# Optimization experiments

Hardware: AMD Instinct MI355X
Metric: run time of the kernel (lower is better)

## Reference

```python
import jax, jax.numpy as jnp
import numpy as np

B, S, VOCAB, E, H, T = 256, 512, 50000, 256, 256, 32
PAD = VOCAB - 1  # mask = sentences != vocab_size - 1 in the original


def setup_inputs() -> dict:
    key = jax.random.key(0)
    ks = jax.random.split(key, 16)
    lengths = jnp.sort(jax.random.randint(ks[0], (B,), S // 2, S + 1))[::-1]
    lengths = lengths.at[0].set(S)  # sorted descending, max length present
    sentences = jax.random.randint(ks[1], (B, S), 0, VOCAB - 1)
    pos = jnp.arange(S)
    sentences = jnp.where(pos[None, :] < lengths[:, None], sentences, PAD)
    tags = jax.random.randint(ks[2], (B, S), 0, T)
    sc = jnp.float32(0.1)
    p = lambda k, shp: jax.random.normal(k, shp, jnp.float32) * sc
    return {
        'embed_table': p(ks[3], (VOCAB + 1, E)),
        'W_ih_f': p(ks[4], (4 * H, E)), 'W_hh_f': p(ks[5], (4 * H, H)),
        'b_ih_f': p(ks[6], (4 * H,)), 'b_hh_f': p(ks[7], (4 * H,)),
        'W_ih_b': p(ks[8], (4 * H, E)), 'W_hh_b': p(ks[9], (4 * H, H)),
        'b_ih_b': p(ks[10], (4 * H,)), 'b_hh_b': p(ks[11], (4 * H,)),
        'W_out': p(ks[12], (T, 2 * H)), 'b_out': p(ks[13], (T,)),
        'transition': jax.random.normal(ks[14], (T, T), jnp.float32),
        'sentences': sentences, 'tags': tags, 'sen_lengths': lengths,
    }


def _run_lstm(x_sbe, W_ih, W_hh, b_ih, b_hh):
    # x_sbe: [S, B, E]; torch gate order i, f, g, o
    Bsz, Hd = x_sbe.shape[1], W_hh.shape[1]
    gx = jnp.einsum('sbe,ge->sbg', x_sbe, W_ih) + b_ih + b_hh  # precompute input gates
    def step(carry, g):
        h, c = carry
        g = g + h @ W_hh.T
        i, f, gg, o = jnp.split(g, 4, axis=-1)
        c = jax.nn.sigmoid(f) * c + jax.nn.sigmoid(i) * jnp.tanh(gg)
        h = jax.nn.sigmoid(o) * jnp.tanh(c)
        return (h, c), h
    h0 = jnp.zeros((Bsz, Hd), x_sbe.dtype)
    _, hs = jax.lax.scan(step, (h0, h0), gx)
    return hs  # [S, B, H]


def _forward(embed_table, W_ih_f, W_hh_f, b_ih_f, b_hh_f,
             W_ih_b, W_hh_b, b_ih_b, b_hh_b, W_out, b_out, transition,
             sentences, tags, sen_lengths):
    mask = sentences != PAD                      # [B, S]
    x = embed_table[sentences]                   # [B, S, E]
    pos = jnp.arange(S)
    valid = pos[None, :] < sen_lengths[:, None]  # [B, S]
    # per-sequence reversal index (packed-sequence-faithful backward direction)
    idx = jnp.where(valid, sen_lengths[:, None] - 1 - pos[None, :], pos[None, :])
    h_f = _run_lstm(x.transpose(1, 0, 2), W_ih_f, W_hh_f, b_ih_f, b_hh_f).transpose(1, 0, 2)
    x_rev = jnp.take_along_axis(x, idx[:, :, None], axis=1)
    h_b = _run_lstm(x_rev.transpose(1, 0, 2), W_ih_b, W_hh_b, b_ih_b, b_hh_b).transpose(1, 0, 2)
    h_b = jnp.take_along_axis(h_b, idx[:, :, None], axis=1)
    h = jnp.concatenate([h_f, h_b], -1) * valid[:, :, None]  # pad_packed pads with zeros
    emit = h @ W_out.T + b_out                   # [B, S, T]; dropout is identity (eval)
    # ---- CRF negative log-likelihood ----
    fmask = mask.astype(emit.dtype)
    real = jnp.take_along_axis(emit, tags[:, :, None], axis=2)[..., 0]  # [B, S]
    real = real.at[:, 1:].add(transition[tags[:, :-1], tags[:, 1:]])
    real_score = (real * fmask).sum(axis=1)      # [B]
    def crf_step(alpha, inp):
        e_i, m_i = inp                           # [B, T], [B]
        scores = alpha[:, :, None] + transition[None, :, :] + e_i[:, None, :]
        new = jax.nn.logsumexp(scores, axis=1)
        return jnp.where(m_i[:, None], new, alpha), None
    alpha0 = emit[:, 0]                          # [B, T]
    xs = (emit[:, 1:].transpose(1, 0, 2), mask[:, 1:].T)
    alpha, _ = jax.lax.scan(crf_step, alpha0, xs)
    log_z = jax.nn.logsumexp(alpha, axis=1)      # [B]
    return -(real_score - log_z)                 # per-example loss [B]


def reference(embed_table, W_ih_f, W_hh_f, b_ih_f, b_hh_f,
              W_ih_b, W_hh_b, b_ih_b, b_hh_b, W_out, b_out, transition,
              sentences, tags, sen_lengths):
    return _forward(embed_table, W_ih_f, W_hh_f, b_ih_f, b_hh_f,
                    W_ih_b, W_hh_b, b_ih_b, b_hh_b, W_out, b_out, transition,
                    sentences, tags, sen_lengths)
```

## Files before the change

### kernel.cpp

```cpp
#include <hip/hip_runtime.h>
#include <hip/hip_bf16.h>


typedef __bf16 bf16x8 __attribute__((ext_vector_type(8)));
typedef float f32x4 __attribute__((ext_vector_type(4)));
typedef unsigned int uint4v __attribute__((ext_vector_type(4)));

__device__ __forceinline__ unsigned short f2bf(float f) {
  union { float f; unsigned int u; } v; v.f = f;
  unsigned int r = v.u + 0x7fffu + ((v.u >> 16) & 1u);
  return (unsigned short)(r >> 16);
}
__device__ __forceinline__ float bf2f(unsigned int lo16) {
  union { unsigned int u; float f; } v; v.u = lo16 << 16;
  return v.f;
}
__device__ __forceinline__ float fsig(float x) {
  float e = __builtin_amdgcn_exp2f(-1.4426950408889634f * x);
  return __builtin_amdgcn_rcpf(1.0f + e);
}
__device__ __forceinline__ float ftanh(float x) {
  float e = __builtin_amdgcn_exp2f(2.8853900817779268f * x);
  return 1.0f - 2.0f * __builtin_amdgcn_rcpf(e + 1.0f);
}

__device__ __forceinline__ void wait_ge(int* p, int target) {
  if (threadIdx.x == 0) {
    while (__hip_atomic_load(p, __ATOMIC_RELAXED, __HIP_MEMORY_SCOPE_AGENT) < target)
      __builtin_amdgcn_s_sleep(2);
    (void)__hip_atomic_load(p, __ATOMIC_ACQUIRE, __HIP_MEMORY_SCOPE_AGENT);
  }
  __syncthreads();
}

__device__ __forceinline__ void lds_barrier() {
  asm volatile("s_waitcnt lgkmcnt(0)\n\ts_barrier" ::: "memory");
}

__global__ void cvt_weights(const float* __restrict__ wih_f, const float* __restrict__ wih_b,
                            const float* __restrict__ whh_f, const float* __restrict__ whh_b,
                            const float* __restrict__ wo,
                            unsigned short* __restrict__ wih,
                            unsigned char* __restrict__ whh8,
                            unsigned char* __restrict__ wout8,
                            int* __restrict__ flags) {
  if (blockIdx.x == 0) {
    for (int f = threadIdx.x; f < 544; f += 256) flags[f] = 0;
  }
  int t = blockIdx.x * 256 + threadIdx.x;
  int i = t * 4;
  if (i < 524288) {
    const float* src = (i < 262144) ? wih_f : wih_b;
    f32x4 v = *(const f32x4*)(src + (i & 262143));
    uint2 p;
    p.x = f2bf(v[0]) | ((unsigned int)f2bf(v[1]) << 16);
    p.y = f2bf(v[2]) | ((unsigned int)f2bf(v[3]) << 16);
    *(uint2*)(wih + i) = p;
  } else if (i < 1048576) {
    int k = i - 524288;
    const float* src = (k < 262144) ? whh_f : whh_b;
    f32x4 v = *(const f32x4*)(src + (k & 262143));
    int r = 0;
    r = __builtin_amdgcn_cvt_pk_fp8_f32(v[0], v[1], r, false);
    r = __builtin_amdgcn_cvt_pk_fp8_f32(v[2], v[3], r, true);
    *(unsigned int*)(whh8 + k) = (unsigned int)r;
  } else if (i < 1064960) {
    int k = i - 1048576;
    f32x4 v = *(const f32x4*)(wo + k);
    int r = 0;
    r = __builtin_amdgcn_cvt_pk_fp8_f32(v[0], v[1], r, false);
    r = __builtin_amdgcn_cvt_pk_fp8_f32(v[2], v[3], r, true);
    *(unsigned int*)(wout8 + k) = (unsigned int)r;
  }
}


__device__ void gemm_role(
    const float* __restrict__ emb, const int* __restrict__ sent, const int* __restrict__ lens,
    const unsigned short* __restrict__ wih,
    const float* __restrict__ bih_f, const float* __restrict__ bhh_f,
    const float* __restrict__ bih_b, const float* __restrict__ bhh_b,
    unsigned short* __restrict__ gx, int* flags,
    unsigned short* wtile, float* btile)
{
  int gb = blockIdx.x - 32;
  int tid = threadIdx.x, w = tid >> 6, lane = tid & 63, col = lane & 15, q = lane >> 4;
  int ns = w >> 2, cg = w & 3;
  int prev_chunk = -1;

  for (int idx = gb; idx < 4096; idx += 224) {
    int k = idx >> 8, t = idx & 255;
    int ss = t >> 6, rest = t & 63;
    int dir = (rest >> 5) & 1, nc = (rest >> 2) & 7, bt = rest & 3;
    if (k != prev_chunk) {
      prev_chunk = k;
      if (k >= 2) wait_ge(&flags[512 + k - 2], 32);
    }
    int n0 = nc * 128, bbase = bt * 64;
    int sbase = k * 32 + ss * 8;

    if (sbase < lens[bbase]) {
      const unsigned short* wsrc = wih + (size_t)dir * 262144;
#pragma unroll
      for (int it = 0; it < 8; it++) {
        int seg = it * 512 + tid;
        int row = seg >> 5, kc = (seg & 31) * 8;
        *(uint4v*)(wtile + row * 264 + kc) = *(const uint4v*)(wsrc + (size_t)(n0 + row) * 256 + kc);
      }
      const float* bi = dir ? bih_b : bih_f;
      const float* bh = dir ? bhh_b : bhh_f;
      if (tid < 128) btile[tid] = bi[n0 + tid] + bh[n0 + tid];
      __syncthreads();

      bf16x8 wf[8][4];
#pragma unroll
      for (int kt = 0; kt < 8; kt++)
#pragma unroll
        for (int nt = 0; nt < 4; nt++)
          wf[kt][nt] = *(const bf16x8*)(wtile + (ns * 64 + nt * 16 + col) * 264 + kt * 32 + q * 8);
      f32x4 bias[4];
#pragma unroll
      for (int nt = 0; nt < 4; nt++)
#pragma unroll
        for (int rr = 0; rr < 4; rr++)
          bias[nt][rr] = btile[ns * 64 + nt * 16 + q * 4 + rr];

      int bidx = bbase + cg * 16 + col;
      int len = lens[bidx];
      const int* srow = sent + bidx * 512;

      for (int i = 0; i < 8; i++) {
        int s = sbase + i;
        int s_eff = dir ? ((s < len) ? (len - 1 - s) : s) : s;
        int token = srow[s_eff];
        const float* ep = emb + (size_t)token * 256;
        bf16x8 xf[8];
#pragma unroll
        for (int kt = 0; kt < 8; kt++) {
          f32x4 a0 = *(const f32x4*)(ep + kt * 32 + q * 8);
          f32x4 a1 = *(const f32x4*)(ep + kt * 32 + q * 8 + 4);
          uint4v pk;
          pk[0] = f2bf(a0[0]) | ((unsigned int)f2bf(a0[1]) << 16);
          pk[1] = f2bf(a0[2]) | ((unsigned int)f2bf(a0[3]) << 16);
          pk[2] = f2bf(a1[0]) | ((unsigned int)f2bf(a1[1]) << 16);
          pk[3] = f2bf(a1[2]) | ((unsigned int)f2bf(a1[3]) << 16);
          xf[kt] = __builtin_bit_cast(bf16x8, pk);
        }
        f32x4 acc[4];
#pragma unroll
        for (int nt = 0; nt < 4; nt++) acc[nt] = bias[nt];
#pragma unroll
        for (int kt = 0; kt < 8; kt++)
#pragma unroll
          for (int nt = 0; nt < 4; nt++)
            acc[nt] = __builtin_amdgcn_mfma_f32_16x16x32_bf16(wf[kt][nt], xf[kt], acc[nt], 0, 0, 0);
        size_t off = (size_t)(k & 1) * 16777216 + (size_t)dir * 8388608
                   + (size_t)(s - k * 32) * 262144 + (size_t)bidx * 1024 + n0 + ns * 64;
#pragma unroll
        for (int nt = 0; nt < 4; nt++) {
          uint2 pk;
          pk.x = f2bf(acc[nt][0]) | ((unsigned int)f2bf(acc[nt][1]) << 16);
          pk.y = f2bf(acc[nt][2]) | ((unsigned int)f2bf(acc[nt][3]) << 16);
          *(uint2*)(gx + off + nt * 16 + q * 4) = pk;
        }
      }
    }
    __syncthreads();
    if (tid == 0)
      __hip_atomic_fetch_add(&flags[k * 32 + ss * 8 + dir * 4 + bt], 1,
                             __ATOMIC_RELEASE, __HIP_MEMORY_SCOPE_AGENT);
  }
}

__device__ void lstm_role(
    const unsigned short* __restrict__ gx,
    const unsigned char* __restrict__ whh8,
    const unsigned char* __restrict__ wout8,
    const float* __restrict__ bout,
    const int* __restrict__ lens,
    unsigned short* __restrict__ emit_f, unsigned short* __restrict__ emit_b,
    int* flags, unsigned char (*hb4)[16 * 264])
{
  int bx = blockIdx.x;
  int dir = bx & 1, grp = bx >> 1, b0 = grp * 16;
  int bt = grp >> 2;
  int tid = threadIdx.x, w = tid >> 6, lane = tid & 63, col = lane & 15, q = lane >> 4;
  int maxlen = lens[b0];
  int bcl = b0 + col;
  int mylen = lens[bcl];

  const unsigned char* whb = whh8 + (size_t)dir * 262144;
  long wh[8][8];
#pragma unroll
  for (int kt = 0; kt < 8; kt++)
#pragma unroll
    for (int t = 0; t < 8; t++) {
      int row0 = (t & 3) * 256 + w * 32 + (t >> 2) * 16;
      wh[kt][t] = *(const long*)(whb + (size_t)(row0 + col) * 256 + kt * 32 + q * 8);
    }

  long wo8[8];
  f32x4 bo4 = (f32x4){0.f, 0.f, 0.f, 0.f};
#pragma unroll
  for (int kt = 0; kt < 8; kt++)
    wo8[kt] = *(const long*)(wout8 + (size_t)((w & 1) * 16 + col) * 512 + dir * 256 + kt * 32 + q * 8);
  if (dir == 0) {
#pragma unroll
    for (int r = 0; r < 4; r++) bo4[r] = bout[(w & 1) * 16 + q * 4 + r];
  }
  unsigned short* ebase = dir ? emit_b : emit_f;

  float c8[8];
  long hf8[8];
#pragma unroll
  for (int i = 0; i < 8; i++) { c8[i] = 0.f; hf8[i] = 0; }

  for (int c = 0; c < 16; c++) {
    int s0 = c * 32;
    if (s0 < maxlen) {
      int cend = s0 + 32; if (cend > maxlen) cend = maxlen;
      const unsigned short* gbase = gx + (size_t)(c & 1) * 16777216 + (size_t)dir * 8388608
                                       + (size_t)bcl * 1024 + q * 4;
      for (int ss = 0; ss < 4; ss++) {
        int sp0 = s0 + ss * 8;
        if (sp0 >= maxlen) break;
        int spe = sp0 + 8; if (spe > cend) spe = cend;
        wait_ge(&flags[c * 32 + ss * 8 + dir * 4 + bt], 8);

        uint2 gxr[8];
        {
          const unsigned short* gf = gbase + (size_t)(sp0 - s0) * 262144;
#pragma unroll
          for (int t = 0; t < 8; t++) {
            int row0 = (t & 3) * 256 + w * 32 + (t >> 2) * 16;
            gxr[t] = *(const uint2*)(gf + row0);
          }
        }

        for (int s = sp0; s < spe; s++) {
          f32x4 acc[8];
#pragma unroll
          for (int t = 0; t < 8; t++) {
            f32x4 a;
            a[0] = bf2f(gxr[t].x & 0xffffu); a[1] = bf2f(gxr[t].x >> 16);
            a[2] = bf2f(gxr[t].y & 0xffffu); a[3] = bf2f(gxr[t].y >> 16);
            acc[t] = a;
          }
          if (s + 1 < spe) {
            const unsigned short* gn = gbase + (size_t)(s + 1 - s0) * 262144;
#pragma unroll
            for (int t = 0; t < 8; t++) {
              int row0 = (t & 3) * 256 + w * 32 + (t >> 2) * 16;
              gxr[t] = *(const uint2*)(gn + row0);
            }
          }
#pragma unroll
          for (int kt = 0; kt < 8; kt++) {
            long hv8 = hf8[kt];
#pragma unroll
            for (int t = 0; t < 8; t++)
              acc[t] = __builtin_amdgcn_mfma_f32_16x16x32_fp8_fp8(wh[kt][t], hv8, acc[t], 0, 0, 0);
          }
          float hv[8];
#pragma unroll
          for (int a = 0; a < 2; a++)
#pragma unroll
            for (int r = 0; r < 4; r++) {
              float ig = acc[a * 4 + 0][r], fg = acc[a * 4 + 1][r];
              float gg = acc[a * 4 + 2][r], og = acc[a * 4 + 3][r];
              float cn = fsig(fg) * c8[a * 4 + r] + fsig(ig) * ftanh(gg);
              c8[a * 4 + r] = cn;
              hv[a * 4 + r] = fsig(og) * ftanh(cn);
            }
          int par = s & 7;
#pragma unroll
          for (int a = 0; a < 2; a++) {
            int r8 = 0;
            r8 = __builtin_amdgcn_cvt_pk_fp8_f32(hv[a * 4 + 0], hv[a * 4 + 1], r8, false);
            r8 = __builtin_amdgcn_cvt_pk_fp8_f32(hv[a * 4 + 2], hv[a * 4 + 3], r8, true);
            *(unsigned int*)(&hb4[par][col * 264 + w * 32 + a * 16 + q * 4]) = (unsigned int)r8;
          }
          lds_barrier();
#pragma unroll
          for (int kt = 0; kt < 8; kt++)
            hf8[kt] = *(const long*)(&hb4[par][col * 264 + kt * 32 + q * 8]);

          if ((s & 3) == 3 || s == spe - 1) {
            int ebeg = s & ~3;
            int e = ebeg + (w >> 1);
            if (e <= s) {
              f32x4 ea = bo4;
#pragma unroll
              for (int kt = 0; kt < 8; kt++) {
                long hbv = *(const long*)(&hb4[e & 7][col * 264 + kt * 32 + q * 8]);
                ea = __builtin_amdgcn_mfma_f32_16x16x32_fp8_fp8(wo8[kt], hbv, ea, 0, 0, 0);
              }
              if (e < mylen) {
                int pos = dir ? (mylen - 1 - e) : e;
                uint2 pk;
                pk.x = f2bf(ea[0]) | ((unsigned int)f2bf(ea[1]) << 16);
                pk.y = f2bf(ea[2]) | ((unsigned int)f2bf(ea[3]) << 16);
                *(uint2*)(ebase + (((size_t)bcl * 512 + pos) * 32 + (w & 1) * 16 + q * 4)) = pk;
              }
            }
          }
        }
      }
    }
    __syncthreads();
    if (tid == 0)
      __hip_atomic_fetch_add(&flags[512 + c], 1, __ATOMIC_RELEASE, __HIP_MEMORY_SCOPE_AGENT);
  }
}

__global__ __launch_bounds__(512, 2) void fused_persist(
    const float* __restrict__ emb, const int* __restrict__ sent, const int* __restrict__ lens,
    const unsigned short* __restrict__ wih,
    const float* __restrict__ bih_f, const float* __restrict__ bhh_f,
    const float* __restrict__ bih_b, const float* __restrict__ bhh_b,
    unsigned short* __restrict__ gx,
    const unsigned char* __restrict__ whh8, const unsigned char* __restrict__ wout8,
    const float* __restrict__ bout,
    unsigned short* __restrict__ emit_f, unsigned short* __restrict__ emit_b,
    int* flags)
{
  __shared__ __align__(16) unsigned short wtile[128 * 264];
  __shared__ __align__(16) float btile[128];
  __shared__ __align__(16) unsigned char hb4[8][16 * 264];

  if (blockIdx.x < 32) {
    lstm_role(gx, whh8, wout8, bout, lens, emit_f, emit_b, flags, hb4);
  } else {
    gemm_role(emb, sent, lens, wih, bih_f, bhh_f, bih_b, bhh_b, gx, flags, wtile, btile);
  }
}

__global__ __launch_bounds__(64) void crf_kernel(
    const unsigned short* __restrict__ emit_f,
    const unsigned short* __restrict__ emit_b,
    const float* __restrict__ trans, const int* __restrict__ tags,
    const int* __restrict__ lens, float* __restrict__ out) {
  const float LOG2E = 1.4426950408889634f, LN2 = 0.6931471805599453f;
  __shared__ __align__(16) float e_lds[512 * 32];
  int b = blockIdx.x, lane = threadIdx.x;
  int len = lens[b];
  const int* tg = tags + b * 512;

  size_t ebase = (size_t)b * 512 * 32;
  const unsigned short* pf = emit_f + ebase;
  const unsigned short* pb = emit_b + ebase;
  int ng = len * 4;
  for (int g = lane; g < ng; g += 64) {
    uint4v fv = *(const uint4v*)(pf + g * 8);
    uint4v bv = *(const uint4v*)(pb + g * 8);
    f32x4 w0, w1;
#pragma unroll
    for (int k = 0; k < 2; k++) {
      w0[2 * k]     = (bf2f(fv[k] & 0xffffu) + bf2f(bv[k] & 0xffffu)) * LOG2E;
      w0[2 * k + 1] = (bf2f(fv[k] >> 16)     + bf2f(bv[k] >> 16))     * LOG2E;
      w1[2 * k]     = (bf2f(fv[k + 2] & 0xffffu) + bf2f(bv[k + 2] & 0xffffu)) * LOG2E;
      w1[2 * k + 1] = (bf2f(fv[k + 2] >> 16)     + bf2f(bv[k + 2] >> 16))     * LOG2E;
    }
    *(f32x4*)(e_lds + g * 8) = w0;
    *(f32x4*)(e_lds + g * 8 + 4) = w1;
  }
  __syncthreads();

  float rs2 = 0.f, rst = 0.f;
  for (int s = lane; s < len; s += 64) {
    int t1 = tg[s];
    rs2 += e_lds[s * 32 + t1];
    if (s > 0) rst += trans[tg[s - 1] * 32 + t1];
  }
  float rsc = LN2 * rs2 + rst;
#pragma unroll
  for (int m = 32; m; m >>= 1) rsc += __shfl_xor(rsc, m);

  int j = lane & 31, half = lane >> 5, i0 = half * 16;
  float tr2[16];
  int pidx[16];
#pragma unroll
  for (int ii = 0; ii < 16; ii++) {
    tr2[ii] = trans[(i0 + ii) * 32 + j] * LOG2E;
    pidx[ii] = (i0 + ii) << 2;
  }
  const float* ep = e_lds + j;
  float B = ep[0];
  float e_nxt = ep[32];
  for (int s = 1; s < len; s++) {
    float e_cur = e_nxt;
    int sn = (s + 1 < len) ? (s + 1) : s;
    e_nxt = ep[sn * 32];
    float v[16];
#pragma unroll
    for (int ii = 0; ii < 16; ii++)
      v[ii] = __builtin_bit_cast(float, __builtin_amdgcn_ds_bpermute(
                  pidx[ii], __builtin_bit_cast(int, B))) + tr2[ii];
    float a8[8], a4[4], a2[2];
#pragma unroll
    for (int ii = 0; ii < 8; ii++) a8[ii] = fmaxf(v[ii], v[ii + 8]);
#pragma unroll
    for (int ii = 0; ii < 4; ii++) a4[ii] = fmaxf(a8[ii], a8[ii + 4]);
    a2[0] = fmaxf(a4[0], a4[2]); a2[1] = fmaxf(a4[1], a4[3]);
    float m1 = fmaxf(a2[0], a2[1]);
    float m2 = fmaxf(m1, __shfl_xor(m1, 32));
    float x[16];
#pragma unroll
    for (int ii = 0; ii < 16; ii++) x[ii] = __builtin_amdgcn_exp2f(v[ii] - m2);
    float s8[8], s4[4], s2[2];
#pragma unroll
    for (int ii = 0; ii < 8; ii++) s8[ii] = x[ii] + x[ii + 8];
#pragma unroll
    for (int ii = 0; ii < 4; ii++) s4[ii] = s8[ii] + s8[ii + 4];
    s2[0] = s4[0] + s4[2]; s2[1] = s4[1] + s4[3];
    float sum = s2[0] + s2[1];
    sum += __shfl_xor(sum, 32);
    B = m2 + __builtin_amdgcn_logf(sum) + e_cur;
  }
  float mz = B;
#pragma unroll
  for (int m = 16; m; m >>= 1) mz = fmaxf(mz, __shfl_xor(mz, m));
  float sz = __builtin_amdgcn_exp2f(B - mz);
#pragma unroll
  for (int m = 16; m; m >>= 1) sz += __shfl_xor(sz, m);
  float logz = LN2 * (mz + __builtin_amdgcn_logf(sz));
  if (lane == 0) out[b] = logz - rsc;
}

extern "C" void kernel_launch(void* const* d_in, const int* in_sizes, int n_in,
                              void* d_out, int out_size, void* d_ws, size_t ws_size,
                              hipStream_t stream) {
  const float* emb   = (const float*)d_in[0];
  const float* Wih_f = (const float*)d_in[1];
  const float* Whh_f = (const float*)d_in[2];
  const float* bih_f = (const float*)d_in[3];
  const float* bhh_f = (const float*)d_in[4];
  const float* Wih_b = (const float*)d_in[5];
  const float* Whh_b = (const float*)d_in[6];
  const float* bih_b = (const float*)d_in[7];
  const float* bhh_b = (const float*)d_in[8];
  const float* Wout  = (const float*)d_in[9];
  const float* bout  = (const float*)d_in[10];
  const float* trans = (const float*)d_in[11];
  const int* sent = (const int*)d_in[12];
  const int* tags = (const int*)d_in[13];
  const int* lens = (const int*)d_in[14];
  float* out = (float*)d_out;

  char* ws = (char*)d_ws;
  if (ws_size < 87048192ull) return;
  unsigned short* gx      = (unsigned short*)(ws);
  unsigned short* emit_f  = (unsigned short*)(ws + 67108864);
  unsigned short* emit_b  = (unsigned short*)(ws + 75497472);
  unsigned short* wih_bf  = (unsigned short*)(ws + 83886080);
  unsigned char*  whh8    = (unsigned char*)(ws + 84934656);
  unsigned char*  wout8   = (unsigned char*)(ws + 85458944);
  int*            flags   = (int*)(ws + 85475328);

  cvt_weights<<<1040, 256, 0, stream>>>(Wih_f, Wih_b, Whh_f, Whh_b, Wout,
                                        wih_bf, whh8, wout8, flags);
  fused_persist<<<256, 512, 0, stream>>>(
      emb, sent, lens, wih_bf, bih_f, bhh_f, bih_b, bhh_b, gx,
      whh8, wout8, bout, emit_f, emit_b, flags);
  crf_kernel<<<256, 64, 0, stream>>>(emit_f, emit_b, trans, tags, lens, out);
}
```

Baseline: 1.545 ms.

## Restructure input-gate GEMM tiles around 16-sequence groups with staged embeddings

The gate-precompute GEMM role now takes a work item covering 16 sequences × 8 steps × all 1024 gate columns for one direction, instead of 64 sequences × 8 steps × 128 columns. Embedding rows are gathered once per tile, converted to bf16 and staged in LDS. Each wave streams its own W_ih fragments directly from global memory in two 64-column passes. Flags become per-LSTM-group, so each LSTM block waits only on its own tile rather than a 64-sequence aggregate. The cost is more global weight traffic per tile (the full 512KB of W_ih per direction is read per tile) and more flag slots to clear and poll.

```diff
diff --git a/kernel.cpp b/kernel.cpp
--- a/kernel.cpp
+++ b/kernel.cpp
@@ -45,7 +45,7 @@
                             unsigned char* __restrict__ wout8,
                             int* __restrict__ flags) {
   if (blockIdx.x == 0) {
-    for (int f = threadIdx.x; f < 544; f += 256) flags[f] = 0;
+    for (int f = threadIdx.x; f < 2080; f += 256) flags[f] = 0;
   }
   int t = blockIdx.x * 256 + threadIdx.x;
   int i = t * 4;
@@ -81,93 +81,105 @@
     const float* __restrict__ bih_f, const float* __restrict__ bhh_f,
     const float* __restrict__ bih_b, const float* __restrict__ bhh_b,
     unsigned short* __restrict__ gx, int* flags,
-    unsigned short* wtile, float* btile)
+    unsigned short* xtile,
+    float* btile)
 {
   int gb = blockIdx.x - 32;
   int tid = threadIdx.x, w = tid >> 6, lane = tid & 63, col = lane & 15, q = lane >> 4;
-  int ns = w >> 2, cg = w & 3;
   int prev_chunk = -1;
 
-  for (int idx = gb; idx < 4096; idx += 224) {
-    int k = idx >> 8, t = idx & 255;
-    int ss = t >> 6, rest = t & 63;
-    int dir = (rest >> 5) & 1, nc = (rest >> 2) & 7, bt = rest & 3;
+  for (int idx = gb; idx < 2048; idx += 224) {
+    int k = idx >> 7, t = idx & 127;
+    int ss = t >> 5, dir = (t >> 4) & 1, sg = t & 15;
     if (k != prev_chunk) {
       prev_chunk = k;
-      if (k >= 2) wait_ge(&flags[512 + k - 2], 32);
+      if (k >= 2) wait_ge(&flags[2048 + k - 2], 32);
     }
-    int n0 = nc * 128, bbase = bt * 64;
+    int b0 = sg * 16;
     int sbase = k * 32 + ss * 8;
 
-    if (sbase < lens[bbase]) {
+    if (sbase < lens[b0]) {
+      {
+        int r = tid >> 2, t4 = tid & 3;
+        int st = r >> 4, si = r & 15;
+        int bidx = b0 + si;
+        int len = lens[bidx];
+        int s = sbase + st;
+        int s_eff = dir ? ((s < len) ? (len - 1 - s) : s) : s;
+        int token = sent[bidx * 512 + s_eff];
+        const float* ep = emb + (size_t)token * 256 + t4 * 64;
+        unsigned short* xd = xtile + r * 264 + t4 * 64;
+#pragma unroll
+        for (int u = 0; u < 4; u++) {
+          f32x4 a0 = *(const f32x4*)(ep + u * 16);
+          f32x4 a1 = *(const f32x4*)(ep + u * 16 + 4);
+          f32x4 a2 = *(const f32x4*)(ep + u * 16 + 8);
+          f32x4 a3 = *(const f32x4*)(ep + u * 16 + 12);
+          uint4v p0, p1;
+          p0[0] = f2bf(a0[0]) | ((unsigned int)f2bf(a0[1]) << 16);
+          p0[1] = f2bf(a0[2]) | ((unsigned int)f2bf(a0[3]) << 16);
+          p0[2] = f2bf(a1[0]) | ((unsigned int)f2bf(a1[1]) << 16);
+          p0[3] = f2bf(a1[2]) | ((unsigned int)f2bf(a1[3]) << 16);
+          p1[0] = f2bf(a2[0]) | ((unsigned int)f2bf(a2[1]) << 16);
+          p1[1] = f2bf(a2[2]) | ((unsigned int)f2bf(a2[3]) << 16);
+          p1[2] = f2bf(a3[0]) | ((unsigned int)f2bf(a3[1]) << 16);
+          p1[3] = f2bf(a3[2]) | ((unsigned int)f2bf(a3[3]) << 16);
+          *(uint4v*)(xd + u * 16) = p0;
+          *(uint4v*)(xd + u * 16 + 8) = p1;
+        }
+        const float* bi = dir ? bih_b : bih_f;
+        const float* bh = dir ? bhh_b : bhh_f;
+        btile[tid] = bi[tid] + bh[tid];
+        btile[tid + 512] = bi[tid + 512] + bh[tid + 512];
+      }
+      __syncthreads();
+
       const unsigned short* wsrc = wih + (size_t)dir * 262144;
 #pragma unroll
-      for (int it = 0; it < 8; it++) {
-        int seg = it * 512 + tid;
-        int row = seg >> 5, kc = (seg & 31) * 8;
-        *(uint4v*)(wtile + row * 264 + kc) = *(const uint4v*)(wsrc + (size_t)(n0 + row) * 256 + kc);
-      }
-      const float* bi = dir ? bih_b : bih_f;
-      const float* bh = dir ? bhh_b : bhh_f;
-      if (tid < 128) btile[tid] = bi[n0 + tid] + bh[n0 + tid];
-      __syncthreads();
-
-      bf16x8 wf[8][4];
-#pragma unroll
-      for (int kt = 0; kt < 8; kt++)
+      for (int ntb = 0; ntb < 2; ntb++) {
+        int gbase = w * 128 + ntb * 64;
+        bf16x8 wf[8][4];
+#pragma unroll
+        for (int kt = 0; kt < 8; kt++)
+#pragma unroll
+          for (int nt = 0; nt < 4; nt++)
+            wf[kt][nt] = *(const bf16x8*)(wsrc + (size_t)(gbase + nt * 16 + col) * 256 + kt * 32 + q * 8);
+        f32x4 bias[4];
 #pragma unroll
         for (int nt = 0; nt < 4; nt++)
-          wf[kt][nt] = *(const bf16x8*)(wtile + (ns * 64 + nt * 16 + col) * 264 + kt * 32 + q * 8);
-      f32x4 bias[4];
-#pragma unroll
-      for (int nt = 0; nt < 4; nt++)
-#pragma unroll
-        for (int rr = 0; rr < 4; rr++)
-          bias[nt][rr] = btile[ns * 64 + nt * 16 + q * 4 + rr];
-
-      int bidx = bbase + cg * 16 + col;
-      int len = lens[bidx];
-      const int* srow = sent + bidx * 512;
-
-      for (int i = 0; i < 8; i++) {
-        int s = sbase + i;
-        int s_eff = dir ? ((s < len) ? (len - 1 - s) : s) : s;
-        int token = srow[s_eff];
-        const float* ep = emb + (size_t)token * 256;
-        bf16x8 xf[8];
-#pragma unroll
-        for (int kt = 0; kt < 8; kt++) {
-          f32x4 a0 = *(const f32x4*)(ep + kt * 32 + q * 8);
-          f32x4 a1 = *(const f32x4*)(ep + kt * 32 + q * 8 + 4);
-          uint4v pk;
-          pk[0] = f2bf(a0[0]) | ((unsigned int)f2bf(a0[1]) << 16);
-          pk[1] = f2bf(a0[2]) | ((unsigned int)f2bf(a0[3]) << 16);
-          pk[2] = f2bf(a1[0]) | ((unsigned int)f2bf(a1[1]) << 16);
-          pk[3] = f2bf(a1[2]) | ((unsigned int)f2bf(a1[3]) << 16);
-          xf[kt] = __builtin_bit_cast(bf16x8, pk);
-        }
-        f32x4 acc[4];
-#pragma unroll
-        for (int nt = 0; nt < 4; nt++) acc[nt] = bias[nt];
-#pragma unroll
-        for (int kt = 0; kt < 8; kt++)
-#pragma unroll
-          for (int nt = 0; nt < 4; nt++)
-            acc[nt] = __builtin_amdgcn_mfma_f32_16x16x32_bf16(wf[kt][nt], xf[kt], acc[nt], 0, 0, 0);
-        size_t off = (size_t)(k & 1) * 16777216 + (size_t)dir * 8388608
-                   + (size_t)(s - k * 32) * 262144 + (size_t)bidx * 1024 + n0 + ns * 64;
-#pragma unroll
-        for (int nt = 0; nt < 4; nt++) {
-          uint2 pk;
-          pk.x = f2bf(acc[nt][0]) | ((unsigned int)f2bf(acc[nt][1]) << 16);
-          pk.y = f2bf(acc[nt][2]) | ((unsigned int)f2bf(acc[nt][3]) << 16);
-          *(uint2*)(gx + off + nt * 16 + q * 4) = pk;
+#pragma unroll
+          for (int rr = 0; rr < 4; rr++)
+            bias[nt][rr] = btile[gbase + nt * 16 + q * 4 + rr];
+
+#pragma unroll
+        for (int st = 0; st < 8; st++) {
+          bf16x8 xf[8];
+#pragma unroll
+          for (int kt = 0; kt < 8; kt++)
+            xf[kt] = *(const bf16x8*)(xtile + (st * 16 + col) * 264 + kt * 32 + q * 8);
+          f32x4 acc[4];
+#pragma unroll
+          for (int nt = 0; nt < 4; nt++) acc[nt] = bias[nt];
+#pragma unroll
+          for (int kt = 0; kt < 8; kt++)
+#pragma unroll
+            for (int nt = 0; nt < 4; nt++)
+              acc[nt] = __builtin_amdgcn_mfma_f32_16x16x32_bf16(wf[kt][nt], xf[kt], acc[nt], 0, 0, 0);
+          size_t off = (size_t)(k & 1) * 16777216 + (size_t)dir * 8388608
+                     + (size_t)(ss * 8 + st) * 262144 + (size_t)(b0 + col) * 1024 + gbase;
+#pragma unroll
+          for (int nt = 0; nt < 4; nt++) {
+            uint2 pk;
+            pk.x = f2bf(acc[nt][0]) | ((unsigned int)f2bf(acc[nt][1]) << 16);
+            pk.y = f2bf(acc[nt][2]) | ((unsigned int)f2bf(acc[nt][3]) << 16);
+            *(uint2*)(gx + off + nt * 16 + q * 4) = pk;
+          }
         }
       }
     }
     __syncthreads();
     if (tid == 0)
-      __hip_atomic_fetch_add(&flags[k * 32 + ss * 8 + dir * 4 + bt], 1,
+      __hip_atomic_fetch_add(&flags[k * 128 + ss * 32 + dir * 16 + sg], 1,
                              __ATOMIC_RELEASE, __HIP_MEMORY_SCOPE_AGENT);
   }
 }
@@ -183,7 +195,6 @@
 {
   int bx = blockIdx.x;
   int dir = bx & 1, grp = bx >> 1, b0 = grp * 16;
-  int bt = grp >> 2;
   int tid = threadIdx.x, w = tid >> 6, lane = tid & 63, col = lane & 15, q = lane >> 4;
   int maxlen = lens[b0];
   int bcl = b0 + col;
@@ -225,7 +236,7 @@
         int sp0 = s0 + ss * 8;
         if (sp0 >= maxlen) break;
         int spe = sp0 + 8; if (spe > cend) spe = cend;
-        wait_ge(&flags[c * 32 + ss * 8 + dir * 4 + bt], 8);
+        wait_ge(&flags[c * 128 + ss * 32 + dir * 16 + grp], 1);
 
         uint2 gxr[8];
         {
@@ -309,7 +320,7 @@
     }
     __syncthreads();
     if (tid == 0)
-      __hip_atomic_fetch_add(&flags[512 + c], 1, __ATOMIC_RELEASE, __HIP_MEMORY_SCOPE_AGENT);
+      __hip_atomic_fetch_add(&flags[2048 + c], 1, __ATOMIC_RELEASE, __HIP_MEMORY_SCOPE_AGENT);
   }
 }
 
@@ -324,14 +335,14 @@
     unsigned short* __restrict__ emit_f, unsigned short* __restrict__ emit_b,
     int* flags)
 {
-  __shared__ __align__(16) unsigned short wtile[128 * 264];
-  __shared__ __align__(16) float btile[128];
+  __shared__ __align__(16) unsigned short xtile[128 * 264];
+  __shared__ __align__(16) float btile[1024];
   __shared__ __align__(16) unsigned char hb4[8][16 * 264];
 
   if (blockIdx.x < 32) {
     lstm_role(gx, whh8, wout8, bout, lens, emit_f, emit_b, flags, hb4);
   } else {
-    gemm_role(emb, sent, lens, wih, bih_f, bhh_f, bih_b, bhh_b, gx, flags, wtile, btile);
+    gemm_role(emb, sent, lens, wih, bih_f, bhh_f, bih_b, bhh_b, gx, flags, xtile, btile);
   }
 }
 
```

New measurement: 1.526 ms. No clear change (-1.2%).
